# Kernel tuning notes

Measured on AMD Instinct MI355X. Metric: run time of the kernel, lower is better.

## Reference

```python
import jax, jax.numpy as jnp
import numpy as np
from jax import lax

N = 100000      # nodes
E = 1600000     # edges
T = 8           # timesteps
DS, DT = 10, 20 # static / temporal features
GH = 64         # gnn_hidden
LH = 64         # lstm_hidden
EC = 64         # end_channels
OC = 1          # out_channels
EPS = 1e-5


def setup_inputs() -> dict:
    key = jax.random.key(0)
    ks = jax.random.split(key, 20)
    g = lambda i, shape, s=0.05: jax.random.normal(ks[i], shape, jnp.float32) * s
    return {
        "x": jax.random.normal(ks[0], (N, DS + DT, T), jnp.float32),
        "edge_index": jax.random.randint(ks[1], (2, E), 0, N, jnp.int64),
        # static encoder (computed in forward but unused downstream, kept for faithfulness)
        "W_static": g(2, (GH, DS)), "b_static": g(3, (GH,)),
        # LSTMCell: input_size = DT + GH, hidden = LH; gate order i,f,g,o
        "W_ih": g(4, (4 * LH, DT + GH)), "W_hh": g(5, (4 * LH, LH)),
        "b_ih": g(6, (4 * LH,)), "b_hh": g(7, (4 * LH,)),
        # GraphConv(lstm_hidden -> gnn_hidden): lin_rel (with bias) on aggregated msgs + lin_root (no bias)
        "W_rel": g(8, (GH, LH)), "b_rel": g(9, (GH,)), "W_root": g(10, (GH, LH)),
        # BatchNorm1d(GH+LH)
        "gamma": jnp.ones((GH + LH,), jnp.float32), "beta": jnp.zeros((GH + LH,), jnp.float32),
        # head: linear1(128->EC), linear2(EC->128), output_layer(128->OC)
        "W1": g(11, (EC, GH + LH)), "b1": g(12, (EC,)),
        "W2": g(13, (GH + LH, EC)), "b2": g(14, (GH + LH,)),
        "W_out": g(15, (OC, GH + LH)), "b_out": g(16, (OC,)),
    }


def reference(x, edge_index, W_static, b_static, W_ih, W_hh, b_ih, b_hh,
              W_rel, b_rel, W_root, gamma, beta, W1, b1, W2, b2, W_out, b_out):
    src, dst = edge_index[0], edge_index[1]
    x_static = x[:, :DS, 0]                      # [N, DS]
    x_temporal = x[:, DS:DS + DT, :]             # [N, DT, T]
    static_embed = x_static @ W_static.T + b_static  # computed but unused (matches source)

    xt_seq = jnp.transpose(x_temporal, (2, 0, 1))  # [T, N, DT]
    h0 = jnp.zeros((N, GH), jnp.float32)
    c0 = jnp.zeros((N, GH), jnp.float32)

    def step(carry, x_t):
        h, c = carry
        # GraphConv: sum-aggregate neighbor h, then linear (linear commutes with sum)
        agg = jax.ops.segment_sum(h[src], dst, num_segments=N)   # [N, LH]
        gnn_out = agg @ W_rel.T + b_rel + h @ W_root.T           # [N, GH]
        inp = jnp.concatenate([x_t, gnn_out], axis=1)            # [N, DT+GH]
        gates = inp @ W_ih.T + b_ih + h @ W_hh.T + b_hh          # [N, 4*LH]
        i, f, g_, o = jnp.split(gates, 4, axis=1)
        c_new = jax.nn.sigmoid(f) * c + jax.nn.sigmoid(i) * jnp.tanh(g_)
        h_new = jax.nn.sigmoid(o) * jnp.tanh(c_new)
        return (h_new, c_new), gnn_out

    (h, c), gnn_outs = lax.scan(step, (h0, c0), xt_seq)
    gnn_out = gnn_outs[-1]  # gnn output computed at the last timestep (pre-update h)

    fused = jnp.concatenate([h, gnn_out], axis=1)                # [N, GH+LH]
    # BatchNorm1d, training-mode batch statistics (dropout p set to 0)
    mean = fused.mean(axis=0)
    var = fused.var(axis=0)
    normed = (fused - mean) * lax.rsqrt(var + EPS) * gamma + beta
    h1 = jax.nn.relu(normed @ W1.T + b1)
    hidden = jax.nn.relu(h1 @ W2.T + b2)
    out = jax.nn.sigmoid(hidden @ W_out.T + b_out)               # binary task -> sigmoid
    return out
```

## Files before the change

### kernel.cpp

```cpp
#include <hip/hip_runtime.h>

#define NN 100000
#define NE 1600000
#define TT 8
#define KF 160
#define XSTR 24
#define NRANGE 8
#define RSPAN 12500
#define CAP 48
#define SCB 50000

typedef __attribute__((ext_vector_type(8))) short bf16x8;
typedef __attribute__((ext_vector_type(4))) float f32x4;
typedef unsigned int uint_;
typedef unsigned short ushort_;
typedef __attribute__((ext_vector_type(4))) uint_ u32x4;

__device__ __forceinline__ float sigf(float x) { return 1.f / (1.f + __expf(-x)); }
__device__ __forceinline__ float tanhf_(float x) { return 1.f - 2.f / (__expf(2.f * x) + 1.f); }
__device__ __forceinline__ ushort_ f2b(float f) {
    uint_ u = __float_as_uint(f);
    u += 0x7fff + ((u >> 16) & 1);
    return (ushort_)(u >> 16);
}
__device__ __forceinline__ float bl(uint_ u) { return __uint_as_float(u << 16); }
__device__ __forceinline__ float bh(uint_ u) { return __uint_as_float(u & 0xffff0000u); }
__device__ __forceinline__ void acc8(float* a, uint4 v) {
    a[0] += bl(v.x); a[1] += bh(v.x); a[2] += bl(v.y); a[3] += bh(v.y);
    a[4] += bl(v.z); a[5] += bh(v.z); a[6] += bl(v.w); a[7] += bh(v.w);
}
__device__ __forceinline__ uint_ pk(float a, float b) {
    return (uint_)f2b(a) | ((uint_)f2b(b) << 16);
}
__device__ __forceinline__ uint4 ntld16(const void* p) {
    u32x4 v = __builtin_nontemporal_load((const u32x4*)p);
    return make_uint4(v[0], v[1], v[2], v[3]);
}

__global__ void k_detect(const int* __restrict__ ei, int* flag) {
    int i = blockIdx.x * 256 + threadIdx.x;
    if (ei[2 * i + 1] != 0) atomicOr(flag, 1);
}

__global__ void k_scxt(const int* __restrict__ ei, const int* __restrict__ flag,
                       int* cnt, int* csr,
                       const float* __restrict__ x, ushort_* __restrict__ xT) {
    __shared__ float xs[32][164];
    int b = blockIdx.x;
    int tid = threadIdx.x;
    if (b < SCB) {
        int range = b & (NRANGE - 1), chunk = b >> 3;
        int e = chunk * 256 + tid;
        if (e >= NE) return;
        int is32 = *flag;
        int d = is32 ? ei[NE + e] : ei[2 * (NE + e)];
        if (d / RSPAN != range) return;
        int s = is32 ? ei[e] : ei[2 * e];
        int pos = atomicAdd(&cnt[d], 1);
        if (pos < CAP) csr[(size_t)d * CAP + pos] = s;
    } else {
        if (!xT) return;
        int nblk = (b - SCB) * 32;
#pragma unroll
        for (int i = 0; i < 5; ++i) {
            int slot = tid + 256 * i;
            int n = slot / 40, f4 = slot - n * 40;
            int n_g = nblk + n;
            float4 v = make_float4(0.f, 0.f, 0.f, 0.f);
            if (n_g < NN) v = *(const float4*)(x + (size_t)n_g * 240 + 80 + f4 * 4);
            *(float4*)(&xs[n][f4 * 4]) = v;
        }
        __syncthreads();
#pragma unroll
        for (int i = 0; i < 3; ++i) {
            int slot = tid + 256 * i;
            int tt = slot / 96, p = slot - tt * 96;
            int n = p / 3, kk0 = (p - n * 3) * 8;
            int n_g = nblk + n;
            if (n_g < NN) {
                uint_ r[4];
#pragma unroll
                for (int u = 0; u < 4; u++) {
                    int k0 = kk0 + u * 2;
                    float f0 = (k0 < 20) ? xs[n][k0 * 8 + tt] : 0.f;
                    float f1 = (k0 + 1 < 20) ? xs[n][(k0 + 1) * 8 + tt] : 0.f;
                    r[u] = pk(f0, f1);
                }
                *(uint4*)(xT + (size_t)tt * NN * XSTR + (size_t)n_g * XSTR + kk0) =
                    make_uint4(r[0], r[1], r[2], r[3]);
            }
        }
    }
}

__global__ void k_prep(const float* __restrict__ W_ih, const float* __restrict__ W_hh,
                       const float* __restrict__ b_ih, const float* __restrict__ b_hh,
                       const float* __restrict__ W_rel, const float* __restrict__ b_rel,
                       const float* __restrict__ W_root, ushort_* WgB, float* bgp) {
    int n = threadIdx.x;
    int k = blockIdx.x;
    if (k < KF) {
        float v = 0.f;
        if (n < 256) {
            int w = n >> 6, g = (n >> 4) & 3, j = w * 16 + (n & 15);
            int row = g * 64 + j;
            if (k < 20) {
                v = W_ih[row * 84 + k];
            } else if (k >= 24 && k < 88) {
                int kk = k - 24;
                float a = 0.f;
                for (int m = 0; m < 64; m++) a += W_ih[row * 84 + 20 + m] * W_rel[m * 64 + kk];
                v = a;
            } else if (k >= 88 && k < 152) {
                int kk = k - 88;
                float a = W_hh[row * 64 + kk];
                for (int m = 0; m < 64; m++) a += W_ih[row * 84 + 20 + m] * W_root[m * 64 + kk];
                v = a;
            }
        } else {
            int j = n - 256;
            if (k >= 24 && k < 88) v = W_rel[j * 64 + (k - 24)];
            else if (k >= 88 && k < 152) v = W_root[j * 64 + (k - 88)];
        }
        WgB[(size_t)n * KF + k] = f2b(v);
    } else {
        if (n < 256) {
            int j = n >> 2, g = n & 3;
            int row = g * 64 + j;
            float a = b_ih[row] + b_hh[row];
            for (int m = 0; m < 64; m++) a += W_ih[row * 84 + 20 + m] * b_rel[m];
            bgp[n] = a;
        } else {
            bgp[n] = b_rel[n - 256];
        }
    }
}

template <bool LAST>
__device__ __forceinline__ void step_body(const float* __restrict__ x,
                                          const ushort_* __restrict__ xT,
                                          const int* __restrict__ cnt,
                                          const int* __restrict__ csr,
                                          const ushort_* __restrict__ hbR,
                                          ushort_* __restrict__ hbW,
                                          float* __restrict__ hf,
                                          float* __restrict__ c,
                                          const ushort_* __restrict__ WgB,
                                          const float* __restrict__ bgp,
                                          float* __restrict__ gnn,
                                          float* __restrict__ sums,
                                          float* __restrict__ sumsq, int t) {
    __shared__ __align__(16) ushort_ Zs[64 * 168];
    __shared__ __align__(16) float Cs0[64 * 64];
    __shared__ int sPerm[64];
    __shared__ int sDeg[64];
    const int tid = threadIdx.x;
    const int nblk = blockIdx.x * 64;
    const int w = tid >> 6, lane = tid & 63;
    const int q = lane >> 4, l16 = lane & 15;

    if (tid < 64) {
        int n_g = nblk + tid;
        int deg = (n_g < NN) ? cnt[n_g] : 0;
        deg = (deg > CAP) ? CAP : deg;
        sDeg[tid] = deg;
        int key = (deg << 6) | tid;
        int rank = 0;
#pragma unroll
        for (int m = 0; m < 64; m++) rank += (__shfl(key, m, 64) > key) ? 1 : 0;
        sPerm[rank] = tid;
    }

#pragma unroll
    for (int i = 0; i < 3; ++i) {
        int slot = tid + 256 * i;
        int n = slot / 12, oo = slot - n * 12;
        int n_g = nblk + n;
        uint4 z = make_uint4(0, 0, 0, 0);
        if (n_g < NN) {
            if (oo < 3) {
                if (xT) {
                    z = ntld16(xT + ((size_t)t * NN + n_g) * XSTR + oo * 8);
                } else {
                    const float* xp = x + (size_t)n_g * 240 + 80 + (size_t)oo * 64 + t;
                    uint_ r[4];
#pragma unroll
                    for (int p = 0; p < 4; p++) {
                        int k0 = oo * 8 + p * 2;
                        ushort_ b0 = (k0 < 20) ? f2b(xp[p * 16]) : (ushort_)0;
                        ushort_ b1 = (k0 + 1 < 20) ? f2b(xp[p * 16 + 8]) : (ushort_)0;
                        r[p] = (uint_)b0 | ((uint_)b1 << 16);
                    }
                    z = make_uint4(r[0], r[1], r[2], r[3]);
                }
            } else if (oo < 11) {
                if (t > 0)
                    z = *(const uint4*)(hbR + (size_t)n_g * 64 + (oo - 3) * 8);
            }
        }
        int oct = (oo < 3) ? oo : ((oo < 11) ? (oo + 8) : 19);
        *(uint4*)(Zs + n * 168 + oct * 8) = z;
    }
    __syncthreads();

    {
        int slot = tid >> 3;
        int l8 = tid & 7;
#pragma unroll
        for (int pass = 0; pass < 2; ++pass) {
            int nn = sPerm[pass ? (63 - slot) : slot];
            float a[8];
#pragma unroll
            for (int i = 0; i < 8; i++) a[i] = 0.f;
            if (t > 0) {
                int deg = sDeg[nn];
                const int* ce = csr + (size_t)(nblk + nn) * CAP;
                int e = 0;
                if (e + 8 <= deg) {
                    uint4 v[8];
#pragma unroll
                    for (int i = 0; i < 8; i++)
                        v[i] = *(const uint4*)(hbR + (size_t)ce[e + i] * 64 + l8 * 8);
                    e += 8;
                    for (; e + 8 <= deg; e += 8) {
#pragma unroll
                        for (int i = 0; i < 4; i++) {
                            acc8(a, v[i]);
                            v[i] = *(const uint4*)(hbR + (size_t)ce[e + i] * 64 + l8 * 8);
                        }
#pragma unroll
                        for (int i = 4; i < 8; i++) {
                            acc8(a, v[i]);
                            v[i] = *(const uint4*)(hbR + (size_t)ce[e + i] * 64 + l8 * 8);
                        }
                    }
#pragma unroll
                    for (int i = 0; i < 8; i++) acc8(a, v[i]);
                }
                for (; e < deg; e++) {
                    uint4 v0 = *(const uint4*)(hbR + (size_t)ce[e] * 64 + l8 * 8);
                    acc8(a, v0);
                }
            }
            uint4 o;
            o.x = pk(a[0], a[1]); o.y = pk(a[2], a[3]);
            o.z = pk(a[4], a[5]); o.w = pk(a[6], a[7]);
            *(uint4*)(Zs + nn * 168 + 24 + l8 * 8) = o;
        }
    }

    if (t > 0) {
        const float* cb = c + (size_t)nblk * 64;
        const int lim = (NN - nblk) * 64;
#pragma unroll
        for (int k2 = 0; k2 < 4; ++k2) {
            int f = (tid + 256 * k2) * 4;
            float4 v = make_float4(0.f, 0.f, 0.f, 0.f);
            if (f < lim) v = *(const float4*)(cb + f);
            *(float4*)(Cs0 + f) = v;
        }
    }
    __syncthreads();

    const int j = w * 16 + l16;
    float sh = 0.f, sh2 = 0.f, sg = 0.f, sg2 = 0.f;

    if (LAST) {
        f32x4 accg[4];
#pragma unroll
        for (int mt = 0; mt < 4; mt++) accg[mt] = (f32x4)(0.f);
#pragma unroll
        for (int kt = 0; kt < 5; ++kt) {
            bf16x8 bfg = *(const bf16x8*)(WgB + (size_t)(256 + w * 16 + l16) * KF + kt * 32 + q * 8);
#pragma unroll
            for (int mt = 0; mt < 4; mt++) {
                bf16x8 af = *(const bf16x8*)(Zs + (mt * 16 + l16) * 168 + kt * 32 + q * 8);
                accg[mt] = __builtin_amdgcn_mfma_f32_16x16x32_bf16(af, bfg, accg[mt], 0, 0, 0);
            }
        }
        const float brl = bgp[256 + j];
#pragma unroll
        for (int mt = 0; mt < 4; ++mt)
#pragma unroll
            for (int r = 0; r < 4; ++r) {
                int node = nblk + mt * 16 + q * 4 + r;
                if (node < NN) {
                    float gn = accg[mt][r] + brl;
                    gnn[(size_t)node * 64 + j] = gn;
                    sg += gn; sg2 += gn * gn;
                }
            }
    }

    f32x4 acc[4][4];
#pragma unroll
    for (int mt = 0; mt < 4; mt++)
#pragma unroll
        for (int nt = 0; nt < 4; nt++) acc[mt][nt] = (f32x4)(0.f);

#pragma unroll
    for (int kt = 0; kt < 5; ++kt) {
        bf16x8 af[4], bf[4];
#pragma unroll
        for (int mt = 0; mt < 4; mt++)
            af[mt] = *(const bf16x8*)(Zs + (mt * 16 + l16) * 168 + kt * 32 + q * 8);
#pragma unroll
        for (int nt = 0; nt < 4; nt++) {
            int n = w * 64 + nt * 16 + l16;
            bf[nt] = *(const bf16x8*)(WgB + (size_t)n * KF + kt * 32 + q * 8);
        }
#pragma unroll
        for (int mt = 0; mt < 4; mt++)
#pragma unroll
            for (int nt = 0; nt < 4; nt++)
                acc[mt][nt] = __builtin_amdgcn_mfma_f32_16x16x32_bf16(af[mt], bf[nt], acc[mt][nt], 0, 0, 0);
    }

    const f32x4 bias = *(const f32x4*)(bgp + j * 4);

    __syncthreads();
    ushort_* Hs   = Zs;
    float*   CsLo = (float*)(Zs + 4096);

    float cnHi[8];
#pragma unroll
    for (int mt = 0; mt < 4; ++mt) {
#pragma unroll
        for (int r = 0; r < 4; ++r) {
            int nloc = mt * 16 + q * 4 + r;
            int node = nblk + nloc;
            float cn = 0.f, hn = 0.f;
            if (node < NN) {
                size_t idx = (size_t)node * 64 + j;
                float iv = sigf(acc[mt][0][r] + bias.x);
                float fv = sigf(acc[mt][1][r] + bias.y);
                float gv = tanhf_(acc[mt][2][r] + bias.z);
                float ov = sigf(acc[mt][3][r] + bias.w);
                float cold = (t > 0) ? Cs0[nloc * 64 + j] : 0.f;
                cn = fv * cold + iv * gv;
                hn = ov * tanhf_(cn);
                if (LAST) {
                    hf[idx] = hn;
                    sh += hn; sh2 += hn * hn;
                }
            }
            Hs[nloc * 64 + j] = f2b(hn);
            if (mt < 2) CsLo[nloc * 64 + j] = cn;
            else        cnHi[(mt - 2) * 4 + r] = cn;
        }
    }
    __syncthreads();
#pragma unroll
    for (int i = 0; i < 2; ++i) {
        int s = tid + 256 * i;
        {
            int n = s >> 3, part = s & 7;
            if (nblk + n < NN)
                *(uint4*)(hbW + (size_t)(nblk + n) * 64 + part * 8) =
                    *(const uint4*)(Hs + n * 64 + part * 8);
        }
        {
            int n = s >> 4, part = s & 15;
            if (nblk + n < NN)
                *(float4*)(c + (size_t)(nblk + n) * 64 + part * 4) =
                    *(const float4*)(CsLo + n * 64 + part * 4);
        }
    }
    __syncthreads();
    float* CsHi = (float*)Zs;
#pragma unroll
    for (int mt = 2; mt < 4; ++mt)
#pragma unroll
        for (int r = 0; r < 4; ++r) {
            int nloc = mt * 16 + q * 4 + r;
            CsHi[(nloc - 32) * 64 + j] = cnHi[(mt - 2) * 4 + r];
        }
    __syncthreads();
#pragma unroll
    for (int i = 0; i < 2; ++i) {
        int s = tid + 256 * i;
        int n = 32 + (s >> 4), part = s & 15;
        if (nblk + n < NN)
            *(float4*)(c + (size_t)(nblk + n) * 64 + part * 4) =
                *(const float4*)(CsHi + (n - 32) * 64 + part * 4);
    }

    if (LAST) {
#pragma unroll
        for (int d = 16; d < 64; d <<= 1) {
            sh += __shfl_xor(sh, d, 64);
            sh2 += __shfl_xor(sh2, d, 64);
            sg += __shfl_xor(sg, d, 64);
            sg2 += __shfl_xor(sg2, d, 64);
        }
        if (q == 0) {
            atomicAdd(&sums[j], sh);
            atomicAdd(&sumsq[j], sh2);
            atomicAdd(&sums[64 + j], sg);
            atomicAdd(&sumsq[64 + j], sg2);
        }
    }
}

__global__ __launch_bounds__(256, 4) void k_step(const float* __restrict__ x,
                                                 const ushort_* __restrict__ xT,
                                                 const int* __restrict__ cnt,
                                                 const int* __restrict__ csr,
                                                 const ushort_* __restrict__ hbR,
                                                 ushort_* __restrict__ hbW,
                                                 float* __restrict__ hf,
                                                 float* __restrict__ c,
                                                 const ushort_* __restrict__ WgB,
                                                 const float* __restrict__ bgp, int t) {
    step_body<false>(x, xT, cnt, csr, hbR, hbW, hf, c, WgB, bgp, nullptr, nullptr, nullptr, t);
}

__global__ __launch_bounds__(256, 4) void k_stepL(const float* __restrict__ x,
                                                  const ushort_* __restrict__ xT,
                                                  const int* __restrict__ cnt,
                                                  const int* __restrict__ csr,
                                                  const ushort_* __restrict__ hbR,
                                                  ushort_* __restrict__ hbW,
                                                  float* __restrict__ hf,
                                                  float* __restrict__ c,
                                                  const ushort_* __restrict__ WgB,
                                                  const float* __restrict__ bgp,
                                                  float* __restrict__ gnn,
                                                  float* __restrict__ sums,
                                                  float* __restrict__ sumsq, int t) {
    step_body<true>(x, xT, cnt, csr, hbR, hbW, hf, c, WgB, bgp, gnn, sums, sumsq, t);
}

__global__ __launch_bounds__(256) void k_head(const float* __restrict__ hf,
                                              const float* __restrict__ gnn,
                                              const float* __restrict__ sums,
                                              const float* __restrict__ sumsq,
                                              const float* __restrict__ gamma,
                                              const float* __restrict__ beta,
                                              const float* __restrict__ W1,
                                              const float* __restrict__ b1,
                                              const float* __restrict__ W2,
                                              const float* __restrict__ b2,
                                              const float* __restrict__ W_out,
                                              const float* __restrict__ b_out,
                                              float* __restrict__ out) {
    __shared__ __align__(16) ushort_ Zs[64 * 168];
    __shared__ __align__(16) ushort_ W1s[64 * 168];
    __shared__ __align__(16) ushort_ W2s[128 * 72];
    __shared__ __align__(16) ushort_ H1s[64 * 72];
    __shared__ float ab[256];
    __shared__ float Obuf[4][64];
    const int tid = threadIdx.x;
    const int w = tid >> 6, lane = tid & 63;
    const int q = lane >> 4, l16 = lane & 15;

    if (tid < 128) {
        float mean = sums[tid] / (float)NN;
        float var = sumsq[tid] / (float)NN - mean * mean;
        float a = gamma[tid] * rsqrtf(var + 1e-5f);
        ab[tid] = a;
        ab[128 + tid] = beta[tid] - mean * a;
    }
#pragma unroll
    for (int i = 0; i < 8; ++i) {
        int slot = tid + 256 * i;
        int jj = slot >> 5, k4 = slot & 31;
        float4 v = *(const float4*)(W1 + (size_t)jj * 128 + k4 * 4);
        *(uint2*)(W1s + jj * 168 + k4 * 4) = make_uint2(pk(v.x, v.y), pk(v.z, v.w));
    }
#pragma unroll
    for (int i = 0; i < 8; ++i) {
        int slot = tid + 256 * i;
        int jj = slot >> 4, k4 = slot & 15;
        float4 v = *(const float4*)(W2 + (size_t)jj * 64 + k4 * 4);
        *(uint2*)(W2s + jj * 72 + k4 * 4) = make_uint2(pk(v.x, v.y), pk(v.z, v.w));
    }
    const int j1 = w * 16 + l16;
    const float bb1 = b1[j1];
    const int j2a = (w * 2) * 16 + l16, j2b = (w * 2 + 1) * 16 + l16;
    const float bb2a = b2[j2a], bb2b = b2[j2b];
    const float woa = W_out[j2a], wob = W_out[j2b];
    const float bo = b_out[0];
    __syncthreads();

    const int NTILE = (NN + 63) / 64;
    for (int tile = blockIdx.x; tile < NTILE; tile += gridDim.x) {
        const int nblk = tile * 64;
#pragma unroll
        for (int i = 0; i < 8; ++i) {
            int slot = tid + 256 * i;
            int n = slot >> 5, f4 = slot & 31;
            int n_g = nblk + n;
            uint2 z = make_uint2(0, 0);
            if (n_g < NN) {
                const float* src = (f4 < 16) ? (hf + (size_t)n_g * 64 + f4 * 4)
                                             : (gnn + (size_t)n_g * 64 + (f4 - 16) * 4);
                float4 v = *(const float4*)src;
                int F = f4 * 4;
                z = make_uint2(pk(v.x * ab[F] + ab[128 + F], v.y * ab[F + 1] + ab[129 + F]),
                               pk(v.z * ab[F + 2] + ab[130 + F], v.w * ab[F + 3] + ab[131 + F]));
            }
            *(uint2*)(Zs + n * 168 + f4 * 4) = z;
        }
        __syncthreads();
        f32x4 acc1[4];
#pragma unroll
        for (int mt = 0; mt < 4; mt++) acc1[mt] = (f32x4)(0.f);
#pragma unroll
        for (int kt = 0; kt < 4; ++kt) {
            bf16x8 bfw = *(const bf16x8*)(W1s + j1 * 168 + kt * 32 + q * 8);
#pragma unroll
            for (int mt = 0; mt < 4; mt++) {
                bf16x8 af = *(const bf16x8*)(Zs + (mt * 16 + l16) * 168 + kt * 32 + q * 8);
                acc1[mt] = __builtin_amdgcn_mfma_f32_16x16x32_bf16(af, bfw, acc1[mt], 0, 0, 0);
            }
        }
#pragma unroll
        for (int mt = 0; mt < 4; mt++)
#pragma unroll
            for (int r = 0; r < 4; r++) {
                int nloc = mt * 16 + q * 4 + r;
                H1s[nloc * 72 + j1] = f2b(fmaxf(acc1[mt][r] + bb1, 0.f));
            }
        __syncthreads();
        f32x4 acc2[4][2];
#pragma unroll
        for (int mt = 0; mt < 4; mt++)
#pragma unroll
            for (int nt = 0; nt < 2; nt++) acc2[mt][nt] = (f32x4)(0.f);
#pragma unroll
        for (int kt = 0; kt < 2; ++kt) {
            bf16x8 bfa = *(const bf16x8*)(W2s + j2a * 72 + kt * 32 + q * 8);
            bf16x8 bfb = *(const bf16x8*)(W2s + j2b * 72 + kt * 32 + q * 8);
#pragma unroll
            for (int mt = 0; mt < 4; mt++) {
                bf16x8 af = *(const bf16x8*)(H1s + (mt * 16 + l16) * 72 + kt * 32 + q * 8);
                acc2[mt][0] = __builtin_amdgcn_mfma_f32_16x16x32_bf16(af, bfa, acc2[mt][0], 0, 0, 0);
                acc2[mt][1] = __builtin_amdgcn_mfma_f32_16x16x32_bf16(af, bfb, acc2[mt][1], 0, 0, 0);
            }
        }
#pragma unroll
        for (int mt = 0; mt < 4; mt++) {
#pragma unroll
            for (int r = 0; r < 4; r++) {
                float p = fmaxf(acc2[mt][0][r] + bb2a, 0.f) * woa +
                          fmaxf(acc2[mt][1][r] + bb2b, 0.f) * wob;
#pragma unroll
                for (int d = 1; d < 16; d <<= 1) p += __shfl_xor(p, d, 64);
                if (l16 == 0) Obuf[w][mt * 16 + q * 4 + r] = p;
            }
        }
        __syncthreads();
        if (tid < 64) {
            int n_g = nblk + tid;
            if (n_g < NN) {
                float s = Obuf[0][tid] + Obuf[1][tid] + Obuf[2][tid] + Obuf[3][tid];
                out[n_g] = sigf(s + bo);
            }
        }
        __syncthreads();
    }
}

extern "C" void kernel_launch(void* const* d_in, const int* in_sizes, int n_in,
                              void* d_out, int out_size, void* d_ws, size_t ws_size,
                              hipStream_t stream) {
    const float* x      = (const float*)d_in[0];
    const int*   ei     = (const int*)d_in[1];
    const float* W_ih   = (const float*)d_in[4];
    const float* W_hh   = (const float*)d_in[5];
    const float* b_ih   = (const float*)d_in[6];
    const float* b_hh   = (const float*)d_in[7];
    const float* W_rel  = (const float*)d_in[8];
    const float* b_rel  = (const float*)d_in[9];
    const float* W_root = (const float*)d_in[10];
    const float* gamma  = (const float*)d_in[11];
    const float* beta   = (const float*)d_in[12];
    const float* W1     = (const float*)d_in[13];
    const float* b1     = (const float*)d_in[14];
    const float* W2     = (const float*)d_in[15];
    const float* b2     = (const float*)d_in[16];
    const float* W_out  = (const float*)d_in[17];
    const float* b_out  = (const float*)d_in[18];
    float* out = (float*)d_out;

    char* ws = (char*)d_ws;
    size_t o = 0;
    auto carve = [&](size_t bytes) { char* p = ws + o; o += (bytes + 255) & ~(size_t)255; return p; };
    int*     cnt   = (int*)carve(NN * 4);
    int*     flag  = (int*)carve(256);
    int*     csr   = (int*)carve((size_t)NN * CAP * 4);
    float*   hf    = (float*)carve((size_t)NN * 64 * 4);
    float*   c     = (float*)carve((size_t)NN * 64 * 4);
    float*   gnn   = (float*)carve((size_t)NN * 64 * 4);
    ushort_* hbA   = (ushort_*)carve((size_t)NN * 64 * 2);
    ushort_* hbB   = (ushort_*)carve((size_t)NN * 64 * 2);
    ushort_* WgB   = (ushort_*)carve((size_t)320 * KF * 2);
    float*   bgp   = (float*)carve(320 * 4);
    float*   sums  = (float*)carve(128 * 4);
    float*   sumsq = (float*)carve(128 * 4);
    ushort_* xT = nullptr;
    size_t need_xt = (size_t)TT * NN * XSTR * 2;
    if (o + need_xt + 256 <= ws_size) xT = (ushort_*)carve(need_xt);

    const int xtb = xT ? (NN + 31) / 32 : 0;

    hipMemsetAsync(flag, 0, 4, stream);
    hipMemsetAsync(cnt, 0, NN * 4, stream);
    k_detect<<<16, 256, 0, stream>>>(ei, flag);
    k_scxt<<<SCB + xtb, 256, 0, stream>>>(ei, flag, cnt, csr, x, xT);

    hipMemsetAsync(sums, 0, 1024, stream);
    k_prep<<<KF + 1, 320, 0, stream>>>(W_ih, W_hh, b_ih, b_hh, W_rel, b_rel, W_root, WgB, bgp);

    const int ngates = (NN + 63) / 64;
    for (int t = 0; t < TT; ++t) {
        ushort_* hbR = (t & 1) ? hbB : hbA;
        ushort_* hbW = (t & 1) ? hbA : hbB;
        if (t == TT - 1)
            k_stepL<<<ngates, 256, 0, stream>>>(x, xT, cnt, csr, hbR, hbW, hf, c,
                                                WgB, bgp, gnn, sums, sumsq, t);
        else
            k_step<<<ngates, 256, 0, stream>>>(x, xT, cnt, csr, hbR, hbW, hf, c,
                                               WgB, bgp, t);
    }

    k_head<<<512, 256, 0, stream>>>(hf, gnn, sums, sumsq, gamma, beta,
                                    W1, b1, W2, b2, W_out, b_out, out);
}
```

Baseline: 847.8 us.

## Fuse first LSTM timestep into CSR-build/transpose kernel and drop t=0 launch

The t=0 step (where h and c are zero, so no graph aggregation is needed) is computed by dedicated blocks interleaved into the CSR-scatter/x-transpose kernel. The separate t=0 step launch is removed and the step kernel drops its t>0 branches. This overlaps the cheap first-step GEMM with the atomic scatter work and removes one launch. In exchange, k_prep must now run before the scatter kernel, and the fused kernel carries extra shared memory and tighter launch bounds.

Result: slower. 1.257 ms (+48.3%).

```diff
diff --git a/kernel.cpp b/kernel.cpp
--- a/kernel.cpp
+++ b/kernel.cpp
@@ -9,6 +9,8 @@
 #define RSPAN 12500
 #define CAP 48
 #define SCB 50000
+#define XTB 3125
+#define NG0 1563
 
 typedef __attribute__((ext_vector_type(8))) short bf16x8;
 typedef __attribute__((ext_vector_type(4))) float f32x4;
@@ -40,57 +42,6 @@
 __global__ void k_detect(const int* __restrict__ ei, int* flag) {
     int i = blockIdx.x * 256 + threadIdx.x;
     if (ei[2 * i + 1] != 0) atomicOr(flag, 1);
-}
-
-__global__ void k_scxt(const int* __restrict__ ei, const int* __restrict__ flag,
-                       int* cnt, int* csr,
-                       const float* __restrict__ x, ushort_* __restrict__ xT) {
-    __shared__ float xs[32][164];
-    int b = blockIdx.x;
-    int tid = threadIdx.x;
-    if (b < SCB) {
-        int range = b & (NRANGE - 1), chunk = b >> 3;
-        int e = chunk * 256 + tid;
-        if (e >= NE) return;
-        int is32 = *flag;
-        int d = is32 ? ei[NE + e] : ei[2 * (NE + e)];
-        if (d / RSPAN != range) return;
-        int s = is32 ? ei[e] : ei[2 * e];
-        int pos = atomicAdd(&cnt[d], 1);
-        if (pos < CAP) csr[(size_t)d * CAP + pos] = s;
-    } else {
-        if (!xT) return;
-        int nblk = (b - SCB) * 32;
-#pragma unroll
-        for (int i = 0; i < 5; ++i) {
-            int slot = tid + 256 * i;
-            int n = slot / 40, f4 = slot - n * 40;
-            int n_g = nblk + n;
-            float4 v = make_float4(0.f, 0.f, 0.f, 0.f);
-            if (n_g < NN) v = *(const float4*)(x + (size_t)n_g * 240 + 80 + f4 * 4);
-            *(float4*)(&xs[n][f4 * 4]) = v;
-        }
-        __syncthreads();
-#pragma unroll
-        for (int i = 0; i < 3; ++i) {
-            int slot = tid + 256 * i;
-            int tt = slot / 96, p = slot - tt * 96;
-            int n = p / 3, kk0 = (p - n * 3) * 8;
-            int n_g = nblk + n;
-            if (n_g < NN) {
-                uint_ r[4];
-#pragma unroll
-                for (int u = 0; u < 4; u++) {
-                    int k0 = kk0 + u * 2;
-                    float f0 = (k0 < 20) ? xs[n][k0 * 8 + tt] : 0.f;
-                    float f1 = (k0 + 1 < 20) ? xs[n][(k0 + 1) * 8 + tt] : 0.f;
-                    r[u] = pk(f0, f1);
-                }
-                *(uint4*)(xT + (size_t)tt * NN * XSTR + (size_t)n_g * XSTR + kk0) =
-                    make_uint4(r[0], r[1], r[2], r[3]);
-            }
-        }
-    }
 }
 
 __global__ void k_prep(const float* __restrict__ W_ih, const float* __restrict__ W_hh,
@@ -136,6 +87,175 @@
     }
 }
 
+__global__ __launch_bounds__(256, 4) void k_scxt0(const int* __restrict__ ei,
+                                                  const int* __restrict__ flag,
+                                                  int* cnt, int* csr,
+                                                  const float* __restrict__ x,
+                                                  ushort_* __restrict__ xT,
+                                                  ushort_* __restrict__ hbW,
+                                                  float* __restrict__ c,
+                                                  const ushort_* __restrict__ WgB,
+                                                  const float* __restrict__ bgp) {
+    __shared__ __align__(16) ushort_ Zs[64 * 168];
+    const int tid = threadIdx.x;
+    const int b = blockIdx.x;
+    const int grp = b >> 5, bpos = b & 31;
+
+    if (bpos == 31 && grp < NG0) {
+        const int nblk = grp * 64;
+        const int w = tid >> 6, lane = tid & 63;
+        const int q = lane >> 4, l16 = lane & 15;
+#pragma unroll
+        for (int i = 0; i < 5; ++i) {
+            int slot = tid + 256 * i;
+            int n = slot / 20, oo = slot - n * 20;
+            int n_g = nblk + n;
+            uint4 z = make_uint4(0, 0, 0, 0);
+            if (n_g < NN && oo < 3) {
+                const float* xp = x + (size_t)n_g * 240 + 80 + (size_t)oo * 64;
+                uint_ rr[4];
+#pragma unroll
+                for (int p = 0; p < 4; p++) {
+                    int k0 = oo * 8 + p * 2;
+                    ushort_ b0 = (k0 < 20) ? f2b(xp[p * 16]) : (ushort_)0;
+                    ushort_ b1 = (k0 + 1 < 20) ? f2b(xp[p * 16 + 8]) : (ushort_)0;
+                    rr[p] = (uint_)b0 | ((uint_)b1 << 16);
+                }
+                z = make_uint4(rr[0], rr[1], rr[2], rr[3]);
+            }
+            *(uint4*)(Zs + n * 168 + oo * 8) = z;
+        }
+        __syncthreads();
+
+        const int j = w * 16 + l16;
+        f32x4 acc[4][4];
+#pragma unroll
+        for (int mt = 0; mt < 4; mt++)
+#pragma unroll
+            for (int nt = 0; nt < 4; nt++) acc[mt][nt] = (f32x4)(0.f);
+        {
+            bf16x8 bf[4];
+#pragma unroll
+            for (int nt = 0; nt < 4; nt++)
+                bf[nt] = *(const bf16x8*)(WgB + (size_t)(w * 64 + nt * 16 + l16) * KF + q * 8);
+#pragma unroll
+            for (int mt = 0; mt < 4; mt++) {
+                bf16x8 af = *(const bf16x8*)(Zs + (mt * 16 + l16) * 168 + q * 8);
+#pragma unroll
+                for (int nt = 0; nt < 4; nt++)
+                    acc[mt][nt] = __builtin_amdgcn_mfma_f32_16x16x32_bf16(af, bf[nt], acc[mt][nt], 0, 0, 0);
+            }
+        }
+
+        const f32x4 bias = *(const f32x4*)(bgp + j * 4);
+        __syncthreads();
+        ushort_* Hs   = Zs;
+        float*   CsLo = (float*)(Zs + 4096);
+        float cnHi[8];
+#pragma unroll
+        for (int mt = 0; mt < 4; ++mt) {
+#pragma unroll
+            for (int r = 0; r < 4; ++r) {
+                int nloc = mt * 16 + q * 4 + r;
+                int node = nblk + nloc;
+                float cn = 0.f, hn = 0.f;
+                if (node < NN) {
+                    float iv = sigf(acc[mt][0][r] + bias.x);
+                    float gv = tanhf_(acc[mt][2][r] + bias.z);
+                    float ov = sigf(acc[mt][3][r] + bias.w);
+                    cn = iv * gv;
+                    hn = ov * tanhf_(cn);
+                }
+                Hs[nloc * 64 + j] = f2b(hn);
+                if (mt < 2) CsLo[nloc * 64 + j] = cn;
+                else        cnHi[(mt - 2) * 4 + r] = cn;
+            }
+        }
+        __syncthreads();
+#pragma unroll
+        for (int i = 0; i < 2; ++i) {
+            int s = tid + 256 * i;
+            {
+                int n = s >> 3, part = s & 7;
+                if (nblk + n < NN)
+                    *(uint4*)(hbW + (size_t)(nblk + n) * 64 + part * 8) =
+                        *(const uint4*)(Hs + n * 64 + part * 8);
+            }
+            {
+                int n = s >> 4, part = s & 15;
+                if (nblk + n < NN)
+                    *(float4*)(c + (size_t)(nblk + n) * 64 + part * 4) =
+                        *(const float4*)(CsLo + n * 64 + part * 4);
+            }
+        }
+        __syncthreads();
+        float* CsHi = (float*)Zs;
+#pragma unroll
+        for (int mt = 2; mt < 4; ++mt)
+#pragma unroll
+            for (int r = 0; r < 4; ++r) {
+                int nloc = mt * 16 + q * 4 + r;
+                CsHi[(nloc - 32) * 64 + j] = cnHi[(mt - 2) * 4 + r];
+            }
+        __syncthreads();
+#pragma unroll
+        for (int i = 0; i < 2; ++i) {
+            int s = tid + 256 * i;
+            int n = 32 + (s >> 4), part = s & 15;
+            if (nblk + n < NN)
+                *(float4*)(c + (size_t)(nblk + n) * 64 + part * 4) =
+                    *(const float4*)(CsHi + (n - 32) * 64 + part * 4);
+        }
+        return;
+    }
+
+    const int r = b - ((grp < NG0) ? grp : NG0);
+    if (r < SCB) {
+        int range = r & (NRANGE - 1), chunk = r >> 3;
+        int e = chunk * 256 + tid;
+        if (e >= NE) return;
+        int is32 = *flag;
+        int d = is32 ? ei[NE + e] : ei[2 * (NE + e)];
+        if (d / RSPAN != range) return;
+        int s = is32 ? ei[e] : ei[2 * e];
+        int pos = atomicAdd(&cnt[d], 1);
+        if (pos < CAP) csr[(size_t)d * CAP + pos] = s;
+    } else {
+        if (!xT) return;
+        float (*xs)[164] = (float (*)[164])Zs;
+        int nblk = (r - SCB) * 32;
+#pragma unroll
+        for (int i = 0; i < 5; ++i) {
+            int slot = tid + 256 * i;
+            int n = slot / 40, f4 = slot - n * 40;
+            int n_g = nblk + n;
+            float4 v = make_float4(0.f, 0.f, 0.f, 0.f);
+            if (n_g < NN) v = *(const float4*)(x + (size_t)n_g * 240 + 80 + f4 * 4);
+            *(float4*)(&xs[n][f4 * 4]) = v;
+        }
+        __syncthreads();
+#pragma unroll
+        for (int i = 0; i < 3; ++i) {
+            int slot = tid + 256 * i;
+            int tt = slot / 96, p = slot - tt * 96;
+            int n = p / 3, kk0 = (p - n * 3) * 8;
+            int n_g = nblk + n;
+            if (n_g < NN) {
+                uint_ rr[4];
+#pragma unroll
+                for (int u = 0; u < 4; u++) {
+                    int k0 = kk0 + u * 2;
+                    float f0 = (k0 < 20) ? xs[n][k0 * 8 + tt] : 0.f;
+                    float f1 = (k0 + 1 < 20) ? xs[n][(k0 + 1) * 8 + tt] : 0.f;
+                    rr[u] = pk(f0, f1);
+                }
+                *(uint4*)(xT + (size_t)tt * NN * XSTR + (size_t)n_g * XSTR + kk0) =
+                    make_uint4(rr[0], rr[1], rr[2], rr[3]);
+            }
+        }
+    }
+}
+
 template <bool LAST>
 __device__ __forceinline__ void step_body(const float* __restrict__ x,
                                           const ushort_* __restrict__ xT,
@@ -194,8 +314,7 @@
                     z = make_uint4(r[0], r[1], r[2], r[3]);
                 }
             } else if (oo < 11) {
-                if (t > 0)
-                    z = *(const uint4*)(hbR + (size_t)n_g * 64 + (oo - 3) * 8);
+                z = *(const uint4*)(hbR + (size_t)n_g * 64 + (oo - 3) * 8);
             }
         }
         int oct = (oo < 3) ? oo : ((oo < 11) ? (oo + 8) : 19);
@@ -212,7 +331,7 @@
             float a[8];
 #pragma unroll
             for (int i = 0; i < 8; i++) a[i] = 0.f;
-            if (t > 0) {
+            {
                 int deg = sDeg[nn];
                 const int* ce = csr + (size_t)(nblk + nn) * CAP;
                 int e = 0;
@@ -249,7 +368,7 @@
         }
     }
 
-    if (t > 0) {
+    {
         const float* cb = c + (size_t)nblk * 64;
         const int lim = (NN - nblk) * 64;
 #pragma unroll
@@ -336,7 +455,7 @@
                 float fv = sigf(acc[mt][1][r] + bias.y);
                 float gv = tanhf_(acc[mt][2][r] + bias.z);
                 float ov = sigf(acc[mt][3][r] + bias.w);
-                float cold = (t > 0) ? Cs0[nloc * 64 + j] : 0.f;
+                float cold = Cs0[nloc * 64 + j];
                 cn = fv * cold + iv * gv;
                 hn = ov * tanhf_(cn);
                 if (LAST) {
@@ -603,18 +722,18 @@
     size_t need_xt = (size_t)TT * NN * XSTR * 2;
     if (o + need_xt + 256 <= ws_size) xT = (ushort_*)carve(need_xt);
 
-    const int xtb = xT ? (NN + 31) / 32 : 0;
-
     hipMemsetAsync(flag, 0, 4, stream);
     hipMemsetAsync(cnt, 0, NN * 4, stream);
+    hipMemsetAsync(sums, 0, 1024, stream);
     k_detect<<<16, 256, 0, stream>>>(ei, flag);
-    k_scxt<<<SCB + xtb, 256, 0, stream>>>(ei, flag, cnt, csr, x, xT);
-
-    hipMemsetAsync(sums, 0, 1024, stream);
     k_prep<<<KF + 1, 320, 0, stream>>>(W_ih, W_hh, b_ih, b_hh, W_rel, b_rel, W_root, WgB, bgp);
 
+    const int xtb = xT ? XTB : 0;
+    k_scxt0<<<SCB + xtb + NG0, 256, 0, stream>>>(ei, flag, cnt, csr, x, xT,
+                                                 hbB, c, WgB, bgp);
+
     const int ngates = (NN + 63) / 64;
-    for (int t = 0; t < TT; ++t) {
+    for (int t = 1; t < TT; ++t) {
         ushort_* hbR = (t & 1) ? hbB : hbA;
         ushort_* hbW = (t & 1) ? hbA : hbB;
         if (t == TT - 1)
```

## Split LSTM gate GEMM into two node halves and drop shared-memory cell-state staging

Applied to the files above, without the earlier changes.

The step kernel now computes the gate GEMM in two 32-node halves, which halves the live accumulator registers. It reads old cell state straight from global memory with nontemporal loads and writes the new cell state directly, instead of staging both through a 16KB shared buffer. Hidden-state staging uses a smaller 32x64 bf16 shared tile, and launch bounds rise from 4 to 5 blocks per SU. The aim is to cut LDS use and registers so occupancy goes up. In exchange, the cell-state writes are now scattered and no longer coalesced as float4, and each half adds extra barriers.

New measurement: 1.303 ms. 53.7% more time.

```diff
diff --git a/kernel.cpp b/kernel.cpp
--- a/kernel.cpp
+++ b/kernel.cpp
@@ -151,7 +151,7 @@
                                           float* __restrict__ sums,
                                           float* __restrict__ sumsq, int t) {
     __shared__ __align__(16) ushort_ Zs[64 * 168];
-    __shared__ __align__(16) float Cs0[64 * 64];
+    __shared__ __align__(16) ushort_ Hs32[32 * 64];
     __shared__ int sPerm[64];
     __shared__ int sDeg[64];
     const int tid = threadIdx.x;
@@ -248,18 +248,6 @@
             *(uint4*)(Zs + nn * 168 + 24 + l8 * 8) = o;
         }
     }
-
-    if (t > 0) {
-        const float* cb = c + (size_t)nblk * 64;
-        const int lim = (NN - nblk) * 64;
-#pragma unroll
-        for (int k2 = 0; k2 < 4; ++k2) {
-            int f = (tid + 256 * k2) * 4;
-            float4 v = make_float4(0.f, 0.f, 0.f, 0.f);
-            if (f < lim) v = *(const float4*)(cb + f);
-            *(float4*)(Cs0 + f) = v;
-        }
-    }
     __syncthreads();
 
     const int j = w * 16 + l16;
@@ -292,97 +280,77 @@
             }
     }
 
-    f32x4 acc[4][4];
-#pragma unroll
-    for (int mt = 0; mt < 4; mt++)
-#pragma unroll
-        for (int nt = 0; nt < 4; nt++) acc[mt][nt] = (f32x4)(0.f);
-
-#pragma unroll
-    for (int kt = 0; kt < 5; ++kt) {
-        bf16x8 af[4], bf[4];
-#pragma unroll
-        for (int mt = 0; mt < 4; mt++)
-            af[mt] = *(const bf16x8*)(Zs + (mt * 16 + l16) * 168 + kt * 32 + q * 8);
-#pragma unroll
-        for (int nt = 0; nt < 4; nt++) {
-            int n = w * 64 + nt * 16 + l16;
-            bf[nt] = *(const bf16x8*)(WgB + (size_t)n * KF + kt * 32 + q * 8);
-        }
-#pragma unroll
-        for (int mt = 0; mt < 4; mt++)
-#pragma unroll
-            for (int nt = 0; nt < 4; nt++)
-                acc[mt][nt] = __builtin_amdgcn_mfma_f32_16x16x32_bf16(af[mt], bf[nt], acc[mt][nt], 0, 0, 0);
-    }
-
     const f32x4 bias = *(const f32x4*)(bgp + j * 4);
 
-    __syncthreads();
-    ushort_* Hs   = Zs;
-    float*   CsLo = (float*)(Zs + 4096);
-
-    float cnHi[8];
-#pragma unroll
-    for (int mt = 0; mt < 4; ++mt) {
-#pragma unroll
-        for (int r = 0; r < 4; ++r) {
-            int nloc = mt * 16 + q * 4 + r;
+#pragma unroll
+    for (int mh = 0; mh < 2; ++mh) {
+        const int nbase = mh * 32;
+        float cold[8];
+#pragma unroll
+        for (int i = 0; i < 8; ++i) {
+            int nloc = nbase + (i >> 2) * 16 + q * 4 + (i & 3);
             int node = nblk + nloc;
-            float cn = 0.f, hn = 0.f;
-            if (node < NN) {
-                size_t idx = (size_t)node * 64 + j;
-                float iv = sigf(acc[mt][0][r] + bias.x);
-                float fv = sigf(acc[mt][1][r] + bias.y);
-                float gv = tanhf_(acc[mt][2][r] + bias.z);
-                float ov = sigf(acc[mt][3][r] + bias.w);
-                float cold = (t > 0) ? Cs0[nloc * 64 + j] : 0.f;
-                cn = fv * cold + iv * gv;
-                hn = ov * tanhf_(cn);
-                if (LAST) {
-                    hf[idx] = hn;
-                    sh += hn; sh2 += hn * hn;
+            cold[i] = (t > 0 && node < NN)
+                          ? __builtin_nontemporal_load(c + (size_t)node * 64 + j)
+                          : 0.f;
+        }
+
+        f32x4 acc[2][4];
+#pragma unroll
+        for (int mt = 0; mt < 2; mt++)
+#pragma unroll
+            for (int nt = 0; nt < 4; nt++) acc[mt][nt] = (f32x4)(0.f);
+
+#pragma unroll
+        for (int kt = 0; kt < 5; ++kt) {
+            bf16x8 af[2], bf[4];
+#pragma unroll
+            for (int mt = 0; mt < 2; mt++)
+                af[mt] = *(const bf16x8*)(Zs + (nbase + mt * 16 + l16) * 168 + kt * 32 + q * 8);
+#pragma unroll
+            for (int nt = 0; nt < 4; nt++) {
+                int n = w * 64 + nt * 16 + l16;
+                bf[nt] = *(const bf16x8*)(WgB + (size_t)n * KF + kt * 32 + q * 8);
+            }
+#pragma unroll
+            for (int mt = 0; mt < 2; mt++)
+#pragma unroll
+                for (int nt = 0; nt < 4; nt++)
+                    acc[mt][nt] = __builtin_amdgcn_mfma_f32_16x16x32_bf16(af[mt], bf[nt], acc[mt][nt], 0, 0, 0);
+        }
+
+#pragma unroll
+        for (int mt = 0; mt < 2; ++mt) {
+#pragma unroll
+            for (int r = 0; r < 4; ++r) {
+                int nloc = nbase + mt * 16 + q * 4 + r;
+                int node = nblk + nloc;
+                float hn = 0.f;
+                if (node < NN) {
+                    size_t idx = (size_t)node * 64 + j;
+                    float iv = sigf(acc[mt][0][r] + bias.x);
+                    float fv = sigf(acc[mt][1][r] + bias.y);
+                    float gv = tanhf_(acc[mt][2][r] + bias.z);
+                    float ov = sigf(acc[mt][3][r] + bias.w);
+                    float cn = fv * cold[mt * 4 + r] + iv * gv;
+                    hn = ov * tanhf_(cn);
+                    c[idx] = cn;
+                    if (LAST) {
+                        hf[idx] = hn;
+                        sh += hn; sh2 += hn * hn;
+                    }
                 }
-            }
-            Hs[nloc * 64 + j] = f2b(hn);
-            if (mt < 2) CsLo[nloc * 64 + j] = cn;
-            else        cnHi[(mt - 2) * 4 + r] = cn;
-        }
-    }
-    __syncthreads();
-#pragma unroll
-    for (int i = 0; i < 2; ++i) {
-        int s = tid + 256 * i;
+                Hs32[(nloc - nbase) * 64 + j] = f2b(hn);
+            }
+        }
+        __syncthreads();
         {
-            int n = s >> 3, part = s & 7;
-            if (nblk + n < NN)
-                *(uint4*)(hbW + (size_t)(nblk + n) * 64 + part * 8) =
-                    *(const uint4*)(Hs + n * 64 + part * 8);
-        }
-        {
-            int n = s >> 4, part = s & 15;
-            if (nblk + n < NN)
-                *(float4*)(c + (size_t)(nblk + n) * 64 + part * 4) =
-                    *(const float4*)(CsLo + n * 64 + part * 4);
-        }
-    }
-    __syncthreads();
-    float* CsHi = (float*)Zs;
-#pragma unroll
-    for (int mt = 2; mt < 4; ++mt)
-#pragma unroll
-        for (int r = 0; r < 4; ++r) {
-            int nloc = mt * 16 + q * 4 + r;
-            CsHi[(nloc - 32) * 64 + j] = cnHi[(mt - 2) * 4 + r];
-        }
-    __syncthreads();
-#pragma unroll
-    for (int i = 0; i < 2; ++i) {
-        int s = tid + 256 * i;
-        int n = 32 + (s >> 4), part = s & 15;
-        if (nblk + n < NN)
-            *(float4*)(c + (size_t)(nblk + n) * 64 + part * 4) =
-                *(const float4*)(CsHi + (n - 32) * 64 + part * 4);
+            int n32 = tid >> 3, part = tid & 7;
+            if (nblk + nbase + n32 < NN)
+                *(uint4*)(hbW + (size_t)(nblk + nbase + n32) * 64 + part * 8) =
+                    *(const uint4*)(Hs32 + n32 * 64 + part * 8);
+        }
+        __syncthreads();
     }
 
     if (LAST) {
@@ -402,7 +370,7 @@
     }
 }
 
-__global__ __launch_bounds__(256, 4) void k_step(const float* __restrict__ x,
+__global__ __launch_bounds__(256, 5) void k_step(const float* __restrict__ x,
                                                  const ushort_* __restrict__ xT,
                                                  const int* __restrict__ cnt,
                                                  const int* __restrict__ csr,
@@ -415,7 +383,7 @@
     step_body<false>(x, xT, cnt, csr, hbR, hbW, hf, c, WgB, bgp, nullptr, nullptr, nullptr, t);
 }
 
-__global__ __launch_bounds__(256, 4) void k_stepL(const float* __restrict__ x,
+__global__ __launch_bounds__(256, 5) void k_stepL(const float* __restrict__ x,
                                                   const ushort_* __restrict__ xT,
                                                   const int* __restrict__ cnt,
                                                   const int* __restrict__ csr,
```
